# Optimization experiments

Hardware: AMD Instinct MI355X
Metric: run time of the kernel (lower is better)

## Reference

```python
import jax, jax.numpy as jnp
import numpy as np

NEG = -1e30  # log(0) surrogate, safe for fp32 logaddexp
BLANK = 0


def setup_inputs() -> dict:
    key = jax.random.key(0)
    k1, k2, k3 = jax.random.split(key, 3)
    T, B, C, S = 1024, 128, 256, 64
    logits = jax.random.normal(k1, (T, B, C), dtype=jnp.float32)
    log_probs = jax.nn.log_softmax(logits, axis=-1)  # CTCLoss expects log-probs
    targets = jax.random.randint(k2, (B, S), 1, C)          # labels in [1, C-1], blank excluded
    target_lengths = jax.random.randint(k3, (B,), 1, S + 1)  # lengths in [1, S]
    return {"log_probs": log_probs, "targets": targets, "target_lengths": target_lengths}


def _ctc_loss(log_probs, targets, target_lengths):
    """CTC loss, blank=0, reduction='mean' (per-sample loss / target_len, then batch mean),
    zero_infinity=True, input_lengths = T for every batch element (as in the wrapper)."""
    T, B, C = log_probs.shape
    S = targets.shape[1]
    L = 2 * S + 1  # extended label length (blanks interleaved)

    # Extended label sequence: [blank, t0, blank, t1, ..., t_{S-1}, blank]  -> (B, L)
    ext = jnp.full((B, L), BLANK, dtype=targets.dtype)
    ext = ext.at[:, 1::2].set(targets)

    # Skip transition (s-2 -> s) allowed iff ext[s] != blank and ext[s] != ext[s-2]
    ext_m2 = jnp.concatenate([jnp.full((B, 2), BLANK, dtype=ext.dtype), ext[:, :-2]], axis=1)
    skip = (ext != BLANK) & (ext != ext_m2)
    skip = skip.at[:, :2].set(False)

    # alpha init at t=0
    lp0 = jnp.take_along_axis(log_probs[0], ext, axis=1)  # (B, L)
    alpha0 = jnp.full((B, L), NEG, dtype=log_probs.dtype)
    alpha0 = alpha0.at[:, 0].set(lp0[:, 0]).at[:, 1].set(lp0[:, 1])

    neg_col = jnp.full((B, 1), NEG, dtype=log_probs.dtype)

    def step(alpha, lp_t):
        lp_ext = jnp.take_along_axis(lp_t, ext, axis=1)            # (B, L)
        p1 = jnp.concatenate([neg_col, alpha[:, :-1]], axis=1)     # alpha[s-1]
        p2 = jnp.concatenate([neg_col, neg_col, alpha[:, :-2]], axis=1)  # alpha[s-2]
        a = jnp.logaddexp(alpha, p1)
        a = jnp.where(skip, jnp.logaddexp(a, p2), a)
        return a + lp_ext, None

    alpha, _ = jax.lax.scan(step, alpha0, log_probs[1:])  # (B, L)

    # Terminal states: s = 2*len and s = 2*len - 1
    idx_last = (2 * target_lengths)[:, None]
    a_last = jnp.take_along_axis(alpha, idx_last, axis=1)[:, 0]
    a_prev = jnp.take_along_axis(alpha, idx_last - 1, axis=1)[:, 0]
    loss = -jnp.logaddexp(a_last, a_prev)  # (B,)

    # zero_infinity=True: infinite (or NEG-saturated) losses -> 0
    loss = jnp.where(jnp.isfinite(loss) & (loss < 1e29), loss, 0.0)

    # reduction='mean': divide each loss by its target length, then mean over batch
    return jnp.mean(loss / target_lengths.astype(loss.dtype))


def reference(log_probs, targets, target_lengths):
    return _ctc_loss(log_probs, targets, target_lengths)
```

## Files before the change

kernel.cpp:

```cpp
#include <hip/hip_runtime.h>
#include <math.h>

#define LOG2E  1.4426950408889634f
#define LN2    0.6931471805599453f

#define T_DIM 1024
#define B_DIM 128
#define C_DIM 256
#define S_DIM 64
#define L_DIM (2 * S_DIM + 1)
#define CH 16
#define NCH (T_DIM / CH)
#define NBUF 6

__device__ __forceinline__ float fexp2(float x) { return __builtin_amdgcn_exp2f(x); }
__device__ __forceinline__ float flog2(float x) { return __builtin_amdgcn_logf(x); }

__device__ __forceinline__ int dpp_shr1_i(int x) {
    return __builtin_amdgcn_update_dpp(0, x, 0x138 , 0xF, 0xF, false);
}

#define GLOAD_LDS16(gp, lp)                                                    \
    __builtin_amdgcn_global_load_lds(                                          \
        (const __attribute__((address_space(1))) void*)(gp),                   \
        (__attribute__((address_space(3))) void*)(lp), 16, 0, 0)

#define VMWAIT(N_) asm volatile("s_waitcnt vmcnt(" #N_ ")" ::: "memory")

__global__ __launch_bounds__(128) void ctc_alpha_kernel(
    const float* __restrict__ log_probs,
    const int* __restrict__ targets,
    const int* __restrict__ target_lengths,
    float* __restrict__ per_batch)
{
    const int b = blockIdx.x;
    const int tid = threadIdx.x;
    const int lane = tid & 63;
    const int wid = tid >> 6;

    __shared__ float rbuf[NBUF][CH][C_DIM];
    __shared__ int prodf;
    __shared__ int consf;

    const int e1 = targets[b * S_DIM + lane];
    const int ep = (lane > 0) ? targets[b * S_DIM + lane - 1] : 0;
    const bool skip = (lane > 0) && (e1 != ep);

    const float* base = log_probs + (size_t)b * C_DIM;
    const size_t stride = (size_t)B_DIM * C_DIM;

    float i0 = base[0];
    float ie = base[e1];
    float a0 = (lane == 0) ? fexp2(i0 * LOG2E) : 0.0f;
    float a1 = (lane == 0) ? fexp2(ie * LOG2E) : 0.0f;
    float a2 = 0.0f;
    int el = 0;
    int dexp = 0;

    if (tid == 0) { prodf = 0; consf = 0; }
    __syncthreads();

#define RESCALE()                                                              \
    do {                                                                       \
        float mx_ = fmaxf(a0, fmaxf(a1, a2));                                  \
        int eb_ = (int)((__float_as_uint(mx_) >> 23) & 0xFFu) - 127;           \
        el += eb_;                                                             \
        float sc_ = __uint_as_float((unsigned)(127 - eb_) << 23);              \
        a0 *= sc_; a1 *= sc_; a2 *= sc_;                                       \
    } while (0)

#define ISSUE_CHUNK(C_, BUF_)                                                  \
    do {                                                                       \
        const int t0_ = 1 + CH * (C_);                                         \
        _Pragma("unroll")                                                      \
        for (int k_ = 0; k_ < CH; ++k_) {                                      \
            int t_ = t0_ + k_;                                                 \
            t_ = (t_ < T_DIM) ? t_ : (T_DIM - 1);                              \
            GLOAD_LDS16(base + (size_t)t_ * stride + 4 * lane,                 \
                        &rbuf[BUF_][k_][0]);                                   \
        }                                                                      \
    } while (0)

#define ACT_STEP(LPB, LPL, K_)                                                 \
    do {                                                                       \
        float pbv_ = fexp2((LPB) * LOG2E);                                     \
        float plv_ = fexp2((LPL) * LOG2E);                                     \
        float am1_ = __int_as_float(dpp_shr1_i(__float_as_int(a1)));           \
        int eprev_ = dpp_shr1_i(el);                                           \
        int iz_ = __float_as_int(a0) | __float_as_int(a1) |                    \
                  __float_as_int(a2);                                          \
        int ele_ = (iz_ == 0) ? eprev_ : el;                                   \
        float am1s_ = ldexpf(am1_, eprev_ - ele_);                             \
        el = ele_;                                                             \
        float n0_ = (a0 + am1s_) * pbv_;                                       \
        float s2_ = skip ? am1s_ : 0.0f;                                       \
        float n1_ = (a1 + a0 + s2_) * plv_;                                    \
        float n2_ = (a2 + a1) * pbv_;                                          \
        a0 = n0_; a1 = n1_; a2 = n2_;                                          \
        if (((K_) & 3) == 3) RESCALE();                                        \
    } while (0)

#define STREAM_STEP(LPB, LPL)                                                  \
    do {                                                                       \
        float pbv_ = fexp2((LPB) * LOG2E);                                     \
        float plv_ = fexp2((LPL) * LOG2E);                                     \
        float am1_ = __int_as_float(dpp_shr1_i(__float_as_int(a1)));           \
        float am1s_ = ldexpf(am1_, dexp);                                      \
        float n0_ = (a0 + am1s_) * pbv_;                                       \
        float s2_ = skip ? am1s_ : 0.0f;                                       \
        float n1_ = (a1 + a0 + s2_) * plv_;                                    \
        float n2_ = (a2 + a1) * pbv_;                                          \
        a0 = n0_; a1 = n1_; a2 = n2_;                                          \
    } while (0)

#define POLL(N_)                                                               \
    do {                                                                       \
        while (*pf < (N_)) { }                                                 \
        __builtin_amdgcn_sched_barrier(0);                                     \
        asm volatile("" ::: "memory");                                         \
    } while (0)

#define GATHER_TO(PLX, PBX, BUF_)                                              \
    do {                                                                       \
        _Pragma("unroll")                                                      \
        for (int k_ = 0; k_ < CH; ++k_) {                                      \
            PLX[k_] = rbuf[BUF_][k_][e1];                                      \
            PBX[k_] = rbuf[BUF_][k_][0];                                       \
        }                                                                      \
    } while (0)

#define ACT_FROM(PLX, PBX)                                                     \
    do {                                                                       \
        _Pragma("unroll")                                                      \
        for (int k_ = 0; k_ < CH; ++k_) {                                      \
            ACT_STEP(PBX[k_], PLX[k_], k_);                                    \
        }                                                                      \
    } while (0)

#define STREAM_FROM(PLX, PBX)                                                  \
    do {                                                                       \
        _Pragma("unroll")                                                      \
        for (int q_ = 0; q_ < 4; ++q_) {                                       \
            dexp = dpp_shr1_i(el) - el;                                        \
            STREAM_STEP(PBX[4 * q_ + 0], PLX[4 * q_ + 0]);                     \
            STREAM_STEP(PBX[4 * q_ + 1], PLX[4 * q_ + 1]);                     \
            STREAM_STEP(PBX[4 * q_ + 2], PLX[4 * q_ + 2]);                     \
            STREAM_STEP(PBX[4 * q_ + 3], PLX[4 * q_ + 3]);                     \
            RESCALE();                                                         \
        }                                                                      \
    } while (0)

#define TAIL_FROM(PLX, PBX)                                                    \
    do {                                                                       \
        _Pragma("unroll")                                                      \
        for (int q_ = 0; q_ < 3; ++q_) {                                       \
            dexp = dpp_shr1_i(el) - el;                                        \
            STREAM_STEP(PBX[4 * q_ + 0], PLX[4 * q_ + 0]);                     \
            STREAM_STEP(PBX[4 * q_ + 1], PLX[4 * q_ + 1]);                     \
            STREAM_STEP(PBX[4 * q_ + 2], PLX[4 * q_ + 2]);                     \
            STREAM_STEP(PBX[4 * q_ + 3], PLX[4 * q_ + 3]);                     \
            RESCALE();                                                         \
        }                                                                      \
        dexp = dpp_shr1_i(el) - el;                                            \
        STREAM_STEP(PBX[12], PLX[12]);                                         \
        STREAM_STEP(PBX[13], PLX[13]);                                         \
        STREAM_STEP(PBX[14], PLX[14]);                                         \
    } while (0)

    if (wid == 1) {
        volatile int* pf = &prodf;
        volatile int* cf = &consf;
        for (int c = 0; c < NCH; ++c) {
            if (c >= NBUF) {
                while (*cf < c - NBUF + 1) __builtin_amdgcn_s_sleep(1);
            }
            ISSUE_CHUNK(c, c % NBUF);
            VMWAIT(32);
            __builtin_amdgcn_sched_barrier(0);
            if (c >= 2 && lane == 0) *pf = c - 1;
        }
        VMWAIT(16);
        __builtin_amdgcn_sched_barrier(0);
        if (lane == 0) *pf = NCH - 1;
        VMWAIT(0);
        __builtin_amdgcn_sched_barrier(0);
        if (lane == 0) *pf = NCH;
    } else {
        volatile int* pf = &prodf;
        volatile int* cf = &consf;
        float plA[CH], pbA[CH], plB[CH], pbB[CH];

        POLL(1);
        GATHER_TO(plA, pbA, 0);
        for (int c = 0; c < 10; c += 2) {
            POLL(c + 2);
            GATHER_TO(plB, pbB, (c + 1) % NBUF);
            ACT_FROM(plA, pbA);
            if (lane == 0) *cf = c + 1;
            POLL(c + 3);
            GATHER_TO(plA, pbA, (c + 2) % NBUF);
            ACT_FROM(plB, pbB);
            if (lane == 0) *cf = c + 2;
        }
        for (int c = 10; c < 62; c += 2) {
            POLL(c + 2);
            GATHER_TO(plB, pbB, (c + 1) % NBUF);
            STREAM_FROM(plA, pbA);
            if (lane == 0) *cf = c + 1;
            POLL(c + 3);
            GATHER_TO(plA, pbA, (c + 2) % NBUF);
            STREAM_FROM(plB, pbB);
            if (lane == 0) *cf = c + 2;
        }
        POLL(NCH);
        GATHER_TO(plB, pbB, (NCH - 1) % NBUF);
        STREAM_FROM(plA, pbA);
        if (lane == 0) *cf = NCH - 1;
        TAIL_FROM(plB, pbB);
        if (lane == 0) *cf = NCH;
    }

#undef TAIL_FROM
#undef STREAM_FROM
#undef ACT_FROM
#undef GATHER_TO
#undef POLL
#undef STREAM_STEP
#undef ACT_STEP
#undef ISSUE_CHUNK
#undef RESCALE

    if (wid == 0) {
        const int len = target_lengths[b];
        float la0 = flog2(a0) + (float)el;
        float la1 = flog2(a1) + (float)el;
        float la2 = flog2(a2) + (float)el;
        float x = (len == S_DIM) ? __shfl(la2, 63, 64) : __shfl(la0, len, 64);
        float y = __shfl(la1, len - 1, 64);
        if (lane == 0) {
            float mx = fmaxf(x, y);
            float lse2 = mx + flog2(1.0f + fexp2(-fabsf(x - y)));
            float loss = -(lse2 * LN2);
            if (!isfinite(loss) || !(loss < 1e29f)) loss = 0.0f;
            per_batch[b] = loss / (float)len;
        }
    }
}

__global__ __launch_bounds__(64) void ctc_reduce_kernel(
    const float* __restrict__ per_batch, float* __restrict__ out)
{
    const int lane = threadIdx.x;
    float v = per_batch[lane] + per_batch[lane + 64];
    #pragma unroll
    for (int off = 32; off > 0; off >>= 1) {
        v += __shfl_down(v, off, 64);
    }
    if (lane == 0) out[0] = v / (float)B_DIM;
}

extern "C" void kernel_launch(void* const* d_in, const int* in_sizes, int n_in,
                              void* d_out, int out_size, void* d_ws, size_t ws_size,
                              hipStream_t stream) {
    const float* log_probs = (const float*)d_in[0];
    const int* targets = (const int*)d_in[1];
    const int* target_lengths = (const int*)d_in[2];
    float* out = (float*)d_out;
    float* per_batch = (float*)d_ws;

    ctc_alpha_kernel<<<B_DIM, 128, 0, stream>>>(log_probs, targets,
                                                target_lengths, per_batch);
    ctc_reduce_kernel<<<1, 64, 0, stream>>>(per_batch, out);
}
```

Before: 51.76 us.

## Add exp-precompute warps between loader and recurrence warp

Launches 256 threads and adds two helper wavefronts that take turns on even and odd chunks. Each one reads the raw log-probs from the LDS ring buffer, computes exp2 of the label and blank values, and writes them as float2 to a second LDS ring. The recurrence wavefront then only gathers already-exponentiated values, which moves the exp work and the indexed LDS gather off its serial critical path. The cost is more LDS, extra handoff flags, and more polling between four wavefronts.

```diff
diff --git a/kernel.cpp b/kernel.cpp
--- a/kernel.cpp
+++ b/kernel.cpp
@@ -11,7 +11,8 @@
 #define L_DIM (2 * S_DIM + 1)
 #define CH 16
 #define NCH (T_DIM / CH)
-#define NBUF 6
+#define RBN 4
+#define PBN 6
 
 __device__ __forceinline__ float fexp2(float x) { return __builtin_amdgcn_exp2f(x); }
 __device__ __forceinline__ float flog2(float x) { return __builtin_amdgcn_logf(x); }
@@ -26,8 +27,12 @@
         (__attribute__((address_space(3))) void*)(lp), 16, 0, 0)
 
 #define VMWAIT(N_) asm volatile("s_waitcnt vmcnt(" #N_ ")" ::: "memory")
-
-__global__ __launch_bounds__(128) void ctc_alpha_kernel(
+#define LGKM0()    asm volatile("s_waitcnt lgkmcnt(0)" ::: "memory")
+#define FENCE()                                                                \
+    do { __builtin_amdgcn_sched_barrier(0);                                    \
+         asm volatile("" ::: "memory"); } while (0)
+
+__global__ __launch_bounds__(256) void ctc_alpha_kernel(
     const float* __restrict__ log_probs,
     const int* __restrict__ targets,
     const int* __restrict__ target_lengths,
@@ -38,8 +43,11 @@
     const int lane = tid & 63;
     const int wid = tid >> 6;
 
-    __shared__ float rbuf[NBUF][CH][C_DIM];
-    __shared__ int prodf;
+    __shared__ float  rbuf[RBN][CH][C_DIM];
+    __shared__ float2 pcv[PBN][CH][64];
+    __shared__ int sf;
+    __shared__ int cvE;
+    __shared__ int cvO;
     __shared__ int consf;
 
     const int e1 = targets[b * S_DIM + lane];
@@ -57,8 +65,13 @@
     int el = 0;
     int dexp = 0;
 
-    if (tid == 0) { prodf = 0; consf = 0; }
+    if (tid == 0) { sf = 0; cvE = 0; cvO = 0; consf = 0; }
     __syncthreads();
+
+    volatile int* vsf = &sf;
+    volatile int* vcE = &cvE;
+    volatile int* vcO = &cvO;
+    volatile int* vcf = &consf;
 
 #define RESCALE()                                                              \
     do {                                                                       \
@@ -81,10 +94,8 @@
         }                                                                      \
     } while (0)
 
-#define ACT_STEP(LPB, LPL, K_)                                                 \
-    do {                                                                       \
-        float pbv_ = fexp2((LPB) * LOG2E);                                     \
-        float plv_ = fexp2((LPL) * LOG2E);                                     \
+#define ACT_STEP(PBV, PLV, K_)                                                 \
+    do {                                                                       \
         float am1_ = __int_as_float(dpp_shr1_i(__float_as_int(a1)));           \
         int eprev_ = dpp_shr1_i(el);                                           \
         int iz_ = __float_as_int(a0) | __float_as_int(a1) |                    \
@@ -92,40 +103,39 @@
         int ele_ = (iz_ == 0) ? eprev_ : el;                                   \
         float am1s_ = ldexpf(am1_, eprev_ - ele_);                             \
         el = ele_;                                                             \
-        float n0_ = (a0 + am1s_) * pbv_;                                       \
+        float n0_ = (a0 + am1s_) * (PBV);                                      \
         float s2_ = skip ? am1s_ : 0.0f;                                       \
-        float n1_ = (a1 + a0 + s2_) * plv_;                                    \
-        float n2_ = (a2 + a1) * pbv_;                                          \
+        float n1_ = (a1 + a0 + s2_) * (PLV);                                   \
+        float n2_ = (a2 + a1) * (PBV);                                         \
         a0 = n0_; a1 = n1_; a2 = n2_;                                          \
         if (((K_) & 3) == 3) RESCALE();                                        \
     } while (0)
 
-#define STREAM_STEP(LPB, LPL)                                                  \
-    do {                                                                       \
-        float pbv_ = fexp2((LPB) * LOG2E);                                     \
-        float plv_ = fexp2((LPL) * LOG2E);                                     \
+#define STREAM_STEP(PBV, PLV)                                                  \
+    do {                                                                       \
         float am1_ = __int_as_float(dpp_shr1_i(__float_as_int(a1)));           \
         float am1s_ = ldexpf(am1_, dexp);                                      \
-        float n0_ = (a0 + am1s_) * pbv_;                                       \
+        float n0_ = (a0 + am1s_) * (PBV);                                      \
         float s2_ = skip ? am1s_ : 0.0f;                                       \
-        float n1_ = (a1 + a0 + s2_) * plv_;                                    \
-        float n2_ = (a2 + a1) * pbv_;                                          \
+        float n1_ = (a1 + a0 + s2_) * (PLV);                                   \
+        float n2_ = (a2 + a1) * (PBV);                                         \
         a0 = n0_; a1 = n1_; a2 = n2_;                                          \
     } while (0)
 
-#define POLL(N_)                                                               \
-    do {                                                                       \
-        while (*pf < (N_)) { }                                                 \
-        __builtin_amdgcn_sched_barrier(0);                                     \
-        asm volatile("" ::: "memory");                                         \
-    } while (0)
-
-#define GATHER_TO(PLX, PBX, BUF_)                                              \
+#define POLLC(C_)                                                              \
+    do {                                                                       \
+        const int cc_ = (C_);                                                  \
+        if (cc_ & 1) { while (*vcO < (cc_ + 1) / 2) { } }                      \
+        else         { while (*vcE < cc_ / 2 + 1) { } }                        \
+        FENCE();                                                               \
+    } while (0)
+
+#define GATHER_TO(PLX, PBX, SLOT)                                              \
     do {                                                                       \
         _Pragma("unroll")                                                      \
         for (int k_ = 0; k_ < CH; ++k_) {                                      \
-            PLX[k_] = rbuf[BUF_][k_][e1];                                      \
-            PBX[k_] = rbuf[BUF_][k_][0];                                       \
+            float2 v_ = pcv[SLOT][k_][lane];                                   \
+            PLX[k_] = v_.x; PBX[k_] = v_.y;                                    \
         }                                                                      \
     } while (0)
 
@@ -168,63 +178,87 @@
     } while (0)
 
     if (wid == 1) {
-        volatile int* pf = &prodf;
-        volatile int* cf = &consf;
         for (int c = 0; c < NCH; ++c) {
-            if (c >= NBUF) {
-                while (*cf < c - NBUF + 1) __builtin_amdgcn_s_sleep(1);
+            if (c >= RBN) {
+                const int d = c - RBN;
+                if (d & 1) { while (*vcO < (d + 1) / 2) __builtin_amdgcn_s_sleep(1); }
+                else       { while (*vcE < d / 2 + 1) __builtin_amdgcn_s_sleep(1); }
+                FENCE();
             }
-            ISSUE_CHUNK(c, c % NBUF);
+            ISSUE_CHUNK(c, c & (RBN - 1));
             VMWAIT(32);
-            __builtin_amdgcn_sched_barrier(0);
-            if (c >= 2 && lane == 0) *pf = c - 1;
+            FENCE();
+            if (c >= 2 && lane == 0) *vsf = c - 1;
         }
         VMWAIT(16);
-        __builtin_amdgcn_sched_barrier(0);
-        if (lane == 0) *pf = NCH - 1;
+        FENCE();
+        if (lane == 0) *vsf = NCH - 1;
         VMWAIT(0);
-        __builtin_amdgcn_sched_barrier(0);
-        if (lane == 0) *pf = NCH;
+        FENCE();
+        if (lane == 0) *vsf = NCH;
+    } else if (wid >= 2) {
+        const int par = wid - 2;
+        for (int c = par; c < NCH; c += 2) {
+            while (*vsf < c + 1) { }
+            if (c >= PBN) {
+                while (*vcf < c - PBN + 1) __builtin_amdgcn_s_sleep(1);
+            }
+            FENCE();
+            const int rb = c & (RBN - 1);
+            const int pb = c % PBN;
+            #pragma unroll
+            for (int k_ = 0; k_ < CH; ++k_) {
+                float pl_ = rbuf[rb][k_][e1];
+                float pb_ = rbuf[rb][k_][0];
+                float2 v_;
+                v_.x = fexp2(pl_ * LOG2E);
+                v_.y = fexp2(pb_ * LOG2E);
+                pcv[pb][k_][lane] = v_;
+            }
+            LGKM0();
+            if (lane == 0) {
+                if (par) *vcO = (c + 1) / 2;
+                else     *vcE = c / 2 + 1;
+            }
+        }
     } else {
-        volatile int* pf = &prodf;
-        volatile int* cf = &consf;
         float plA[CH], pbA[CH], plB[CH], pbB[CH];
 
-        POLL(1);
+        POLLC(0);
         GATHER_TO(plA, pbA, 0);
         for (int c = 0; c < 10; c += 2) {
-            POLL(c + 2);
-            GATHER_TO(plB, pbB, (c + 1) % NBUF);
+            POLLC(c + 1);
+            GATHER_TO(plB, pbB, (c + 1) % PBN);
             ACT_FROM(plA, pbA);
-            if (lane == 0) *cf = c + 1;
-            POLL(c + 3);
-            GATHER_TO(plA, pbA, (c + 2) % NBUF);
+            if (lane == 0) *vcf = c + 1;
+            POLLC(c + 2);
+            GATHER_TO(plA, pbA, (c + 2) % PBN);
             ACT_FROM(plB, pbB);
-            if (lane == 0) *cf = c + 2;
+            if (lane == 0) *vcf = c + 2;
         }
         for (int c = 10; c < 62; c += 2) {
-            POLL(c + 2);
-            GATHER_TO(plB, pbB, (c + 1) % NBUF);
+            POLLC(c + 1);
+            GATHER_TO(plB, pbB, (c + 1) % PBN);
             STREAM_FROM(plA, pbA);
-            if (lane == 0) *cf = c + 1;
-            POLL(c + 3);
-            GATHER_TO(plA, pbA, (c + 2) % NBUF);
+            if (lane == 0) *vcf = c + 1;
+            POLLC(c + 2);
+            GATHER_TO(plA, pbA, (c + 2) % PBN);
             STREAM_FROM(plB, pbB);
-            if (lane == 0) *cf = c + 2;
-        }
-        POLL(NCH);
-        GATHER_TO(plB, pbB, (NCH - 1) % NBUF);
+            if (lane == 0) *vcf = c + 2;
+        }
+        POLLC(NCH - 1);
+        GATHER_TO(plB, pbB, (NCH - 1) % PBN);
         STREAM_FROM(plA, pbA);
-        if (lane == 0) *cf = NCH - 1;
+        if (lane == 0) *vcf = NCH - 1;
         TAIL_FROM(plB, pbB);
-        if (lane == 0) *cf = NCH;
+        if (lane == 0) *vcf = NCH;
     }
 
 #undef TAIL_FROM
 #undef STREAM_FROM
 #undef ACT_FROM
 #undef GATHER_TO
-#undef POLL
+#undef POLLC
 #undef STREAM_STEP
 #undef ACT_STEP
 #undef ISSUE_CHUNK
@@ -268,7 +302,7 @@
     float* out = (float*)d_out;
     float* per_batch = (float*)d_ws;
 
-    ctc_alpha_kernel<<<B_DIM, 128, 0, stream>>>(log_probs, targets,
+    ctc_alpha_kernel<<<B_DIM, 256, 0, stream>>>(log_probs, targets,
                                                 target_lengths, per_batch);
     ctc_reduce_kernel<<<1, 64, 0, stream>>>(per_batch, out);
 }
```

Result: faster. 45.83 us (-11.5%).
